# Performance work log

Hardware: AMD Instinct MI355X
Metric: run time of the kernel (lower is better)

Reference implementation:

```python
import jax, jax.numpy as jnp
import numpy as np

N_NODES = 100000
N_EDGES = 1600000
D_IN = 128
D_OUT = 128
K_HOPS = 2


def gcn_norm(edge_index, num_nodes):
    # Add self-loops (weight 1), compute symmetric normalization
    # norm_e = deg^{-1/2}[src] * deg^{-1/2}[dst], deg over destination index.
    loop = jnp.arange(num_nodes, dtype=edge_index.dtype)
    src = jnp.concatenate([edge_index[0], loop])
    dst = jnp.concatenate([edge_index[1], loop])
    w = jnp.ones(src.shape[0], dtype=jnp.float32)
    deg = jax.ops.segment_sum(w, dst, num_segments=num_nodes)
    dinv = jnp.where(deg > 0, jax.lax.rsqrt(deg), 0.0)
    norm = dinv[src] * dinv[dst]
    return src, dst, norm


def setup_inputs() -> dict:
    key = jax.random.key(0)
    k1, k2, k3, k4 = jax.random.split(key, 4)
    x = jax.random.normal(k1, (N_NODES, D_IN), dtype=jnp.float32)
    edge_index = jax.random.randint(k2, (2, N_EDGES), 0, N_NODES, dtype=jnp.int64)
    # SGConv linear params (Glorot-ish scale)
    W = jax.random.normal(k3, (D_IN, D_OUT), dtype=jnp.float32) / np.sqrt(D_IN)
    b = jnp.zeros((D_OUT,), dtype=jnp.float32)
    return {"x": x, "edge_index": edge_index, "W": W, "b": b}


def reference(x, edge_index, W, b):
    n = x.shape[0]
    src, dst, norm = gcn_norm(edge_index, n)
    h = x
    for _ in range(K_HOPS):
        # gather source features, scale by edge norm, scatter-add to destinations
        h = jax.ops.segment_sum(h[src] * norm[:, None], dst, num_segments=n)
    return h @ W + b
```

## Files before the change

kernel.cpp:

```cpp
#include <hip/hip_runtime.h>
#include <hip/hip_bf16.h>


#define DFEAT 128
#define ELLW 64
#define ABLK 2048
#define CAP 4608
#define NBUCKMAX 512

typedef __attribute__((ext_vector_type(8))) short short8;
typedef __attribute__((ext_vector_type(4))) float f32x4;
typedef __attribute__((ext_vector_type(4))) unsigned int u32x4;
typedef __attribute__((ext_vector_type(4))) int i32x4;

__device__ __forceinline__ float bf2f(unsigned short u) {
    union { unsigned int i; float f; } t;
    t.i = ((unsigned int)u) << 16;
    return t.f;
}

__device__ __forceinline__ unsigned short f2bf(float f) {
    union { float f; unsigned int i; } t;
    t.f = f;
    unsigned int lsb = (t.i >> 16) & 1u;
    t.i += 0x7fffu + lsb;
    return (unsigned short)(t.i >> 16);
}

__device__ __forceinline__ void accum8(float* acc, uint4 u, float w) {
    acc[0] += bf2f((unsigned short)(u.x & 0xffffu)) * w;
    acc[1] += bf2f((unsigned short)(u.x >> 16)) * w;
    acc[2] += bf2f((unsigned short)(u.y & 0xffffu)) * w;
    acc[3] += bf2f((unsigned short)(u.y >> 16)) * w;
    acc[4] += bf2f((unsigned short)(u.z & 0xffffu)) * w;
    acc[5] += bf2f((unsigned short)(u.z >> 16)) * w;
    acc[6] += bf2f((unsigned short)(u.w & 0xffffu)) * w;
    acc[7] += bf2f((unsigned short)(u.w >> 16)) * w;
}

__device__ __forceinline__ void add8(float* acc, uint4 u) {
    union { unsigned int i; float f; } a;
    a.i = u.x << 16;          acc[0] += a.f;
    a.i = u.x & 0xffff0000u;  acc[1] += a.f;
    a.i = u.y << 16;          acc[2] += a.f;
    a.i = u.y & 0xffff0000u;  acc[3] += a.f;
    a.i = u.z << 16;          acc[4] += a.f;
    a.i = u.z & 0xffff0000u;  acc[5] += a.f;
    a.i = u.w << 16;          acc[6] += a.f;
    a.i = u.w & 0xffff0000u;  acc[7] += a.f;
}

__global__ void k_detect(const unsigned short* __restrict__ xs,
                         const int* __restrict__ ei, int* __restrict__ flags) {
    int t = blockIdx.x * 256 + (int)threadIdx.x;
    int bad = 0;
    for (int i = t; i < 16384; i += 2048) {
        unsigned int e = (xs[i] >> 7) & 0xFFu;
        if (e >= 0xC0u) bad = 1;
    }
    if (__any(bad) && (threadIdx.x & 63) == 0) atomicOr(flags, 1);
    int oddnz = 0;
    for (int i = t; i < 4096; i += 2048) {
        if (ei[2 * i + 1] != 0) oddnz = 1;
    }
    if (__any(oddnz) && (threadIdx.x & 63) == 0) atomicOr(flags + 1, 1);
}

__global__ void k_prepB(const void* __restrict__ Wraw, const int* __restrict__ flags,
                        unsigned short* __restrict__ Bf) {
    int t = blockIdx.x * 256 + threadIdx.x;
    if (t >= 2048) return;
    int lane = t & 63;
    int chunk = (t >> 6) & 3;
    int ntile = t >> 8;
    int ncol = ntile * 16 + (lane & 15);
    int k0 = chunk * 32 + (lane >> 4) * 8;
    int isf = flags[0];
    const float* Wf = (const float*)Wraw;
    const unsigned short* Wb = (const unsigned short*)Wraw;
    unsigned short* o = Bf + (size_t)t * 8;
#pragma unroll
    for (int j = 0; j < 8; j++) {
        int idx = (k0 + j) * DFEAT + ncol;
        o[j] = isf ? f2bf(Wf[idx]) : Wb[idx];
    }
}

__global__ __launch_bounds__(256) void k_bucketA(const int* __restrict__ ei, int E, int n,
                                                 const int* __restrict__ flags,
                                                 int* __restrict__ bucketCnt,
                                                 unsigned int* __restrict__ buck) {
    __shared__ int sdst[ABLK];
    __shared__ int ssrc[ABLK];
    __shared__ int hist[NBUCKMAX];
    __shared__ int base_[NBUCKMAX];
    int tid = (int)threadIdx.x;
    for (int t = tid; t < NBUCKMAX; t += 256) hist[t] = 0;
    __syncthreads();
    int e0 = blockIdx.x * ABLK;
    int i64 = (flags[1] == 0);

    if (e0 + ABLK <= E) {
        int d[8], s[8];
#pragma unroll
        for (int k = 0; k < 8; k++) {
            int e = e0 + tid + k * 256;
            d[k] = i64 ? __builtin_nontemporal_load(ei + 2 * (E + e))
                       : __builtin_nontemporal_load(ei + E + e);
        }
#pragma unroll
        for (int k = 0; k < 8; k++) {
            int e = e0 + tid + k * 256;
            s[k] = i64 ? __builtin_nontemporal_load(ei + 2 * e)
                       : __builtin_nontemporal_load(ei + e);
        }
#pragma unroll
        for (int k = 0; k < 8; k++) {
            sdst[tid + k * 256] = d[k];
            ssrc[tid + k * 256] = s[k];
            atomicAdd(&hist[d[k] >> 8], 1);
        }
    } else {
        for (int e = e0 + tid; e < E; e += 256) {
            int d = i64 ? ei[2 * (E + e)] : ei[E + e];
            int s = i64 ? ei[2 * e] : ei[e];
            sdst[e - e0] = d;
            ssrc[e - e0] = s;
            atomicAdd(&hist[d >> 8], 1);
        }
    }
    __syncthreads();
#pragma unroll
    for (int r = 0; r < 2; r++) {
        int t = (tid + r * 256 + (int)blockIdx.x * 61) & (NBUCKMAX - 1);
        int cc = hist[t];
        base_[t] = cc ? atomicAdd(bucketCnt + t, cc) : 0;
        hist[t] = 0;
    }
    __syncthreads();
    int nloc = min(ABLK, E - e0);
    if (nloc == ABLK) {
#pragma unroll
        for (int k = 0; k < 8; k++) {
            int idx = tid + k * 256;
            int d = sdst[idx], s = ssrc[idx];
            int b = d >> 8;
            int pos = base_[b] + atomicAdd(&hist[b], 1);
            if (pos < CAP)
                buck[(size_t)b * CAP + pos] =
                    (unsigned int)s | ((unsigned int)(d & 255) << 17);
        }
    } else {
        for (int idx = tid; idx < nloc; idx += 256) {
            int d = sdst[idx], s = ssrc[idx];
            int b = d >> 8;
            int pos = base_[b] + atomicAdd(&hist[b], 1);
            if (pos < CAP)
                buck[(size_t)b * CAP + pos] =
                    (unsigned int)s | ((unsigned int)(d & 255) << 17);
        }
    }
}

__global__ __launch_bounds__(256) void k_bucketB_gemm0(
        const unsigned int* __restrict__ buck,
        const int* __restrict__ bucketCnt, int n,
        int* __restrict__ cnt, int* __restrict__ ell,
        const void* __restrict__ xraw,
        const unsigned short* __restrict__ Bf,
        const int* __restrict__ flags,
        unsigned short* __restrict__ g0) {
    __shared__ int lcnt[256];
    __shared__ unsigned short thi[16 * 136];
    __shared__ unsigned short tlo[16 * 136];
    int b = blockIdx.x;
    int tid = (int)threadIdx.x;
    lcnt[tid] = 0;
    __syncthreads();

    int m0 = min(bucketCnt[b], CAP);
    int node0 = b << 8;
    const unsigned int* bp = buck + (size_t)b * CAP;
    for (int base = 0; base < m0; base += 1024) {
        unsigned int w[4];
#pragma unroll
        for (int j = 0; j < 4; j++) {
            int i = base + tid + j * 256;
            w[j] = (i < m0) ? __builtin_nontemporal_load(bp + i) : 0xFFFFFFFFu;
        }
#pragma unroll
        for (int j = 0; j < 4; j++) {
            if (w[j] != 0xFFFFFFFFu) {
                int s = (int)(w[j] & 0x1FFFFu);
                int dl = (int)(w[j] >> 17);
                int pos = atomicAdd(&lcnt[dl], 1);
                if (pos < ELLW) ell[(size_t)(node0 + dl) * ELLW + pos] = s;
            }
        }
    }
    __syncthreads();
    {
        int node = node0 + tid;
        if (node < n) {
            int c = lcnt[tid];
            cnt[node] = c;
            int st = min(c, ELLW);
            int slots = min((c + 16) & ~15, ELLW);
            int* rowp = ell + (size_t)node * ELLW;
            for (int p = st; p < slots; p++) rowp[p] = node;
        }
    }

    int isf = flags[0];
    int wave = tid >> 6;
    int lane = tid & 63;
    int g = lane >> 4, c = lane & 15;
    int trow = wave * 4 + g;

    for (int tile = 0; tile < 16; ++tile) {
        int lrow = tile * 16 + trow;
        int node = node0 + lrow;
        uint4 ohi = {0, 0, 0, 0}, olo = {0, 0, 0, 0};
        if (node < n) {
            if (isf) {
                const float* xf = (const float*)xraw;
                f32x4 v0 = __builtin_nontemporal_load((const f32x4*)(xf + (size_t)node * DFEAT + c * 8));
                f32x4 v1 = __builtin_nontemporal_load((const f32x4*)(xf + (size_t)node * DFEAT + c * 8 + 4));
                float vv[8] = {v0[0], v0[1], v0[2], v0[3], v1[0], v1[1], v1[2], v1[3]};
                unsigned short h[8], l[8];
#pragma unroll
                for (int j = 0; j < 8; j++) {
                    h[j] = f2bf(vv[j]);
                    l[j] = f2bf(vv[j] - bf2f(h[j]));
                }
                ohi.x = (unsigned int)h[0] | ((unsigned int)h[1] << 16);
                ohi.y = (unsigned int)h[2] | ((unsigned int)h[3] << 16);
                ohi.z = (unsigned int)h[4] | ((unsigned int)h[5] << 16);
                ohi.w = (unsigned int)h[6] | ((unsigned int)h[7] << 16);
                olo.x = (unsigned int)l[0] | ((unsigned int)l[1] << 16);
                olo.y = (unsigned int)l[2] | ((unsigned int)l[3] << 16);
                olo.z = (unsigned int)l[4] | ((unsigned int)l[5] << 16);
                olo.w = (unsigned int)l[6] | ((unsigned int)l[7] << 16);
            } else {
                u32x4 u = __builtin_nontemporal_load(
                    (const u32x4*)((const unsigned short*)xraw + (size_t)node * DFEAT + c * 8));
                ohi.x = u[0]; ohi.y = u[1]; ohi.z = u[2]; ohi.w = u[3];
            }
        }
        __syncthreads();
        *(uint4*)(thi + trow * 136 + c * 8) = ohi;
        *(uint4*)(tlo + trow * 136 + c * 8) = olo;
        __syncthreads();

        int m = c, quad = g;
        f32x4 acc2[2];
        acc2[0] = (f32x4){0.f, 0.f, 0.f, 0.f};
        acc2[1] = (f32x4){0.f, 0.f, 0.f, 0.f};
#pragma unroll
        for (int c2 = 0; c2 < 4; c2++) {
            short8 ah = *(const short8*)(thi + m * 136 + c2 * 32 + quad * 8);
            short8 al = *(const short8*)(tlo + m * 136 + c2 * 32 + quad * 8);
#pragma unroll
            for (int t = 0; t < 2; t++) {
                int nt = wave * 2 + t;
                short8 bfr = *(const short8*)(Bf + ((size_t)(nt * 4 + c2) * 64 + lane) * 8);
                acc2[t] = __builtin_amdgcn_mfma_f32_16x16x32_bf16(ah, bfr, acc2[t], 0, 0, 0);
                acc2[t] = __builtin_amdgcn_mfma_f32_16x16x32_bf16(al, bfr, acc2[t], 0, 0, 0);
            }
        }

        float sc[4];
#pragma unroll
        for (int r2 = 0; r2 < 4; r2++) {
            int lr = tile * 16 + quad * 4 + r2;
            sc[r2] = (node0 + lr < n) ? rsqrtf((float)(lcnt[lr] + 1)) : 0.f;
        }
#pragma unroll
        for (int t = 0; t < 2; t++) {
            int col = (wave * 2 + t) * 16 + m;
#pragma unroll
            for (int r2 = 0; r2 < 4; r2++) {
                int gnode = node0 + tile * 16 + quad * 4 + r2;
                if (gnode < n)
                    g0[(size_t)gnode * DFEAT + col] = f2bf(acc2[t][r2] * sc[r2]);
            }
        }
    }
}

__device__ __forceinline__ void hop_accum(const unsigned short* __restrict__ fb,
                                          const int* __restrict__ ell,
                                          int node, int cn, int lane, float* acc) {
    int g = lane >> 4, c = lane & 15;
    int slots = min((cn + 16) & ~15, ELLW);
    const int* row = ell + (size_t)node * ELLW;
#pragma unroll
    for (int j = 0; j < 8; j++) acc[j] = 0.f;

    for (int base = 0; base < slots; base += 16) {
        i32x4 s4 = __builtin_nontemporal_load((const i32x4*)(row + base) + g);
        uint4 u0 = *(const uint4*)(fb + (size_t)s4[0] * DFEAT + c * 8);
        uint4 u1 = *(const uint4*)(fb + (size_t)s4[1] * DFEAT + c * 8);
        uint4 u2 = *(const uint4*)(fb + (size_t)s4[2] * DFEAT + c * 8);
        uint4 u3 = *(const uint4*)(fb + (size_t)s4[3] * DFEAT + c * 8);
        add8(acc, u0);
        add8(acc, u1);
        add8(acc, u2);
        add8(acc, u3);
    }
    float corrw = (cn < ELLW) ? (float)(cn + 1 - slots) : 1.0f;
    if (g == 0 && corrw != 0.0f) {
        uint4 u = *(const uint4*)(fb + (size_t)node * DFEAT + c * 8);
        accum8(acc, u, corrw);
    }
#pragma unroll
    for (int j = 0; j < 8; j++) {
        acc[j] += __shfl_xor(acc[j], 16);
        acc[j] += __shfl_xor(acc[j], 32);
    }
}

__global__ __launch_bounds__(256) void k_hop(const unsigned short* __restrict__ src,
                                             const int* __restrict__ ell,
                                             const int* __restrict__ cnt,
                                             unsigned short* __restrict__ outb, int n) {
    int node = blockIdx.x * 4 + (threadIdx.x >> 6);
    if (node >= n) return;
    int lane = threadIdx.x & 63;
    int cn = cnt[node];
    float acc[8];
    hop_accum(src, ell, node, cn, lane, acc);
    if ((lane >> 4) == 0) {
        int c = lane & 15;
        float sc = 1.0f / (float)(cn + 1);
        uint4 o;
        o.x = (unsigned int)f2bf(acc[0] * sc) | ((unsigned int)f2bf(acc[1] * sc) << 16);
        o.y = (unsigned int)f2bf(acc[2] * sc) | ((unsigned int)f2bf(acc[3] * sc) << 16);
        o.z = (unsigned int)f2bf(acc[4] * sc) | ((unsigned int)f2bf(acc[5] * sc) << 16);
        o.w = (unsigned int)f2bf(acc[6] * sc) | ((unsigned int)f2bf(acc[7] * sc) << 16);
        *(uint4*)(outb + (size_t)node * DFEAT + c * 8) = o;
    }
}

__global__ __launch_bounds__(256) void k_hop2_out(const unsigned short* __restrict__ src,
                                                  const int* __restrict__ ell,
                                                  const int* __restrict__ cnt,
                                                  const void* __restrict__ braw,
                                                  const int* __restrict__ flags,
                                                  void* __restrict__ outraw, int n) {
    int node = blockIdx.x * 4 + (threadIdx.x >> 6);
    if (node >= n) return;
    int lane = threadIdx.x & 63;
    int cn = cnt[node];
    float acc[8];
    hop_accum(src, ell, node, cn, lane, acc);
    if ((lane >> 4) == 0) {
        int c = lane & 15;
        float sc = rsqrtf((float)(cn + 1));
        int isf = flags[0];
        const float* bf32 = (const float*)braw;
        const unsigned short* bb16 = (const unsigned short*)braw;
#pragma unroll
        for (int j = 0; j < 8; j++) {
            float bias = isf ? bf32[c * 8 + j] : bf2f(bb16[c * 8 + j]);
            acc[j] = acc[j] * sc + bias;
        }
        if (isf) {
            float* outf = (float*)outraw;
            *(float4*)(outf + (size_t)node * DFEAT + c * 8) =
                (float4){acc[0], acc[1], acc[2], acc[3]};
            *(float4*)(outf + (size_t)node * DFEAT + c * 8 + 4) =
                (float4){acc[4], acc[5], acc[6], acc[7]};
        } else {
            unsigned short* outb = (unsigned short*)outraw;
            uint4 o;
            o.x = (unsigned int)f2bf(acc[0]) | ((unsigned int)f2bf(acc[1]) << 16);
            o.y = (unsigned int)f2bf(acc[2]) | ((unsigned int)f2bf(acc[3]) << 16);
            o.z = (unsigned int)f2bf(acc[4]) | ((unsigned int)f2bf(acc[5]) << 16);
            o.w = (unsigned int)f2bf(acc[6]) | ((unsigned int)f2bf(acc[7]) << 16);
            *(uint4*)(outb + (size_t)node * DFEAT + c * 8) = o;
        }
    }
}

extern "C" void kernel_launch(void* const* d_in, const int* in_sizes, int n_in,
                              void* d_out, int out_size, void* d_ws, size_t ws_size,
                              hipStream_t stream) {
    const void* x = d_in[0];
    const int* ei = (const int*)d_in[1];
    const void* W = d_in[2];
    const void* b = d_in[3];

    const int n = in_sizes[0] / DFEAT;
    const int E = in_sizes[1] / 2;

    int* ell = (int*)d_ws;
    unsigned short* g1 = (unsigned short*)(ell + (size_t)n * ELLW);
    int* cnt = (int*)(g1 + (size_t)n * DFEAT);
    int* flags = cnt + n;
    int* bucketCnt = flags + 4;
    unsigned short* Bf = (unsigned short*)(bucketCnt + NBUCKMAX);
    unsigned short* g0 = (unsigned short*)d_out;
    unsigned int* buck = (unsigned int*)g1;

    (void)hipMemsetAsync(flags, 0, (4 + NBUCKMAX) * sizeof(int), stream);

    k_detect<<<8, 256, 0, stream>>>((const unsigned short*)x, ei, flags);

    k_prepB<<<8, 256, 0, stream>>>(W, flags, Bf);

    int nbuck = (n + 255) >> 8;
    int ablocks = (E + ABLK - 1) / ABLK;
    k_bucketA<<<ablocks, 256, 0, stream>>>(ei, E, n, flags, bucketCnt, buck);

    k_bucketB_gemm0<<<nbuck, 256, 0, stream>>>(buck, bucketCnt, n, cnt, ell,
                                               x, Bf, flags, g0);

    k_hop<<<(n + 3) / 4, 256, 0, stream>>>(g0, ell, cnt, g1, n);

    k_hop2_out<<<(n + 3) / 4, 256, 0, stream>>>(g1, ell, cnt, b, flags, d_out, n);
}
```

Baseline: 308.1 us.

## Locally sort edges by bucket before scatter and merge setup kernels

The bucketing kernel now processes 4096 edges per block, builds a per-block prefix scan over bucket histograms, and locally sorts edge indices by destination bucket in shared memory. Global writes to bucket arrays then become contiguous runs per bucket, which should coalesce better. Separately, the memset, dtype-detect and W-prep launches are merged into a single one-block setup kernel to cut launch overhead. The cost is more shared-memory passes and barriers, plus fewer resident blocks from the larger LDS footprint.

Result: slower. 324.7 us (+5.4%).

```diff
diff --git a/kernel.cpp b/kernel.cpp
--- a/kernel.cpp
+++ b/kernel.cpp
@@ -4,7 +4,7 @@
 
 #define DFEAT 128
 #define ELLW 64
-#define ABLK 2048
+#define ABLK 4096
 #define CAP 4608
 #define NBUCKMAX 512
 
@@ -50,39 +50,46 @@
     a.i = u.w & 0xffff0000u;  acc[7] += a.f;
 }
 
-__global__ void k_detect(const unsigned short* __restrict__ xs,
-                         const int* __restrict__ ei, int* __restrict__ flags) {
-    int t = blockIdx.x * 256 + (int)threadIdx.x;
+__global__ __launch_bounds__(256) void k_setup(const unsigned short* __restrict__ xs,
+                                               const int* __restrict__ ei,
+                                               const void* __restrict__ Wraw,
+                                               int* __restrict__ flags,
+                                               int* __restrict__ bucketCnt,
+                                               unsigned short* __restrict__ Bf) {
+    __shared__ int s_f32, s_odd;
+    int tid = (int)threadIdx.x;
+    if (tid == 0) { s_f32 = 0; s_odd = 0; }
+    for (int i = tid; i < NBUCKMAX; i += 256) bucketCnt[i] = 0;
+    __syncthreads();
     int bad = 0;
-    for (int i = t; i < 16384; i += 2048) {
+    for (int i = tid; i < 16384; i += 256) {
         unsigned int e = (xs[i] >> 7) & 0xFFu;
         if (e >= 0xC0u) bad = 1;
     }
-    if (__any(bad) && (threadIdx.x & 63) == 0) atomicOr(flags, 1);
-    int oddnz = 0;
-    for (int i = t; i < 4096; i += 2048) {
-        if (ei[2 * i + 1] != 0) oddnz = 1;
-    }
-    if (__any(oddnz) && (threadIdx.x & 63) == 0) atomicOr(flags + 1, 1);
-}
-
-__global__ void k_prepB(const void* __restrict__ Wraw, const int* __restrict__ flags,
-                        unsigned short* __restrict__ Bf) {
-    int t = blockIdx.x * 256 + threadIdx.x;
-    if (t >= 2048) return;
-    int lane = t & 63;
-    int chunk = (t >> 6) & 3;
-    int ntile = t >> 8;
-    int ncol = ntile * 16 + (lane & 15);
-    int k0 = chunk * 32 + (lane >> 4) * 8;
-    int isf = flags[0];
+    if (bad) atomicOr(&s_f32, 1);
+    int odd = 0;
+    for (int i = tid; i < 4096; i += 256) {
+        if (ei[2 * i + 1] != 0) odd = 1;
+    }
+    if (odd) atomicOr(&s_odd, 1);
+    __syncthreads();
+    int isf = s_f32;
+    if (tid == 0) { flags[0] = s_f32; flags[1] = s_odd; }
+
     const float* Wf = (const float*)Wraw;
     const unsigned short* Wb = (const unsigned short*)Wraw;
-    unsigned short* o = Bf + (size_t)t * 8;
-#pragma unroll
-    for (int j = 0; j < 8; j++) {
-        int idx = (k0 + j) * DFEAT + ncol;
-        o[j] = isf ? f2bf(Wf[idx]) : Wb[idx];
+    for (int t = tid; t < 2048; t += 256) {
+        int lane = t & 63;
+        int chunk = (t >> 6) & 3;
+        int ntile = t >> 8;
+        int ncol = ntile * 16 + (lane & 15);
+        int k0 = chunk * 32 + (lane >> 4) * 8;
+        unsigned short* o = Bf + (size_t)t * 8;
+#pragma unroll
+        for (int j = 0; j < 8; j++) {
+            int idx = (k0 + j) * DFEAT + ncol;
+            o[j] = isf ? f2bf(Wf[idx]) : Wb[idx];
+        }
     }
 }
 
@@ -90,75 +97,74 @@
                                                  const int* __restrict__ flags,
                                                  int* __restrict__ bucketCnt,
                                                  unsigned int* __restrict__ buck) {
-    __shared__ int sdst[ABLK];
+    __shared__ int sd[ABLK];
     __shared__ int ssrc[ABLK];
+    __shared__ unsigned short sidx[ABLK];
     __shared__ int hist[NBUCKMAX];
-    __shared__ int base_[NBUCKMAX];
+    __shared__ int loff[NBUCKMAX];
+    __shared__ int gbase[NBUCKMAX];
+    __shared__ int cur[NBUCKMAX];
+    __shared__ int scan_s[256];
+
     int tid = (int)threadIdx.x;
     for (int t = tid; t < NBUCKMAX; t += 256) hist[t] = 0;
     __syncthreads();
     int e0 = blockIdx.x * ABLK;
+    int nloc = min(ABLK, E - e0);
     int i64 = (flags[1] == 0);
 
-    if (e0 + ABLK <= E) {
-        int d[8], s[8];
-#pragma unroll
-        for (int k = 0; k < 8; k++) {
-            int e = e0 + tid + k * 256;
-            d[k] = i64 ? __builtin_nontemporal_load(ei + 2 * (E + e))
-                       : __builtin_nontemporal_load(ei + E + e);
-        }
-#pragma unroll
-        for (int k = 0; k < 8; k++) {
-            int e = e0 + tid + k * 256;
-            s[k] = i64 ? __builtin_nontemporal_load(ei + 2 * e)
-                       : __builtin_nontemporal_load(ei + e);
-        }
-#pragma unroll
-        for (int k = 0; k < 8; k++) {
-            sdst[tid + k * 256] = d[k];
-            ssrc[tid + k * 256] = s[k];
-            atomicAdd(&hist[d[k] >> 8], 1);
-        }
-    } else {
-        for (int e = e0 + tid; e < E; e += 256) {
-            int d = i64 ? ei[2 * (E + e)] : ei[E + e];
-            int s = i64 ? ei[2 * e] : ei[e];
-            sdst[e - e0] = d;
-            ssrc[e - e0] = s;
-            atomicAdd(&hist[d >> 8], 1);
-        }
-    }
-    __syncthreads();
+    for (int i = tid; i < nloc; i += 256) {
+        int e = e0 + i;
+        int d = i64 ? __builtin_nontemporal_load(ei + 2 * (E + e))
+                    : __builtin_nontemporal_load(ei + E + e);
+        int s = i64 ? __builtin_nontemporal_load(ei + 2 * e)
+                    : __builtin_nontemporal_load(ei + e);
+        sd[i] = d;
+        ssrc[i] = s;
+    }
+    __syncthreads();
+
+    for (int i = tid; i < nloc; i += 256) atomicAdd(&hist[sd[i] >> 8], 1);
+    __syncthreads();
+
+    int a0 = hist[2 * tid], a1 = hist[2 * tid + 1];
+    int pair = a0 + a1;
+    scan_s[tid] = pair;
+    __syncthreads();
+    for (int off = 1; off < 256; off <<= 1) {
+        int t = (tid >= off) ? scan_s[tid - off] : 0;
+        __syncthreads();
+        scan_s[tid] += t;
+        __syncthreads();
+    }
+    int ex = scan_s[tid] - pair;
+    loff[2 * tid] = ex;
+    loff[2 * tid + 1] = ex + a0;
+
 #pragma unroll
     for (int r = 0; r < 2; r++) {
         int t = (tid + r * 256 + (int)blockIdx.x * 61) & (NBUCKMAX - 1);
         int cc = hist[t];
-        base_[t] = cc ? atomicAdd(bucketCnt + t, cc) : 0;
-        hist[t] = 0;
-    }
-    __syncthreads();
-    int nloc = min(ABLK, E - e0);
-    if (nloc == ABLK) {
-#pragma unroll
-        for (int k = 0; k < 8; k++) {
-            int idx = tid + k * 256;
-            int d = sdst[idx], s = ssrc[idx];
-            int b = d >> 8;
-            int pos = base_[b] + atomicAdd(&hist[b], 1);
-            if (pos < CAP)
-                buck[(size_t)b * CAP + pos] =
-                    (unsigned int)s | ((unsigned int)(d & 255) << 17);
-        }
-    } else {
-        for (int idx = tid; idx < nloc; idx += 256) {
-            int d = sdst[idx], s = ssrc[idx];
-            int b = d >> 8;
-            int pos = base_[b] + atomicAdd(&hist[b], 1);
-            if (pos < CAP)
-                buck[(size_t)b * CAP + pos] =
-                    (unsigned int)s | ((unsigned int)(d & 255) << 17);
-        }
+        gbase[t] = cc ? atomicAdd(bucketCnt + t, cc) : 0;
+        cur[t] = 0;
+    }
+    __syncthreads();
+
+    for (int i = tid; i < nloc; i += 256) {
+        int b = sd[i] >> 8;
+        int p = loff[b] + atomicAdd(&cur[b], 1);
+        sidx[p] = (unsigned short)i;
+    }
+    __syncthreads();
+
+    for (int i = tid; i < nloc; i += 256) {
+        int idx = sidx[i];
+        int d = sd[idx];
+        int b = d >> 8;
+        int pos = gbase[b] + (i - loff[b]);
+        if (pos < CAP)
+            buck[(size_t)b * CAP + pos] =
+                (unsigned int)ssrc[idx] | ((unsigned int)(d & 255) << 17);
     }
 }
 
@@ -403,11 +409,8 @@
     unsigned short* g0 = (unsigned short*)d_out;
     unsigned int* buck = (unsigned int*)g1;
 
-    (void)hipMemsetAsync(flags, 0, (4 + NBUCKMAX) * sizeof(int), stream);
-
-    k_detect<<<8, 256, 0, stream>>>((const unsigned short*)x, ei, flags);
-
-    k_prepB<<<8, 256, 0, stream>>>(W, flags, Bf);
+    k_setup<<<1, 256, 0, stream>>>((const unsigned short*)x, ei, W,
+                                   flags, bucketCnt, Bf);
 
     int nbuck = (n + 255) >> 8;
     int ablocks = (E + ABLK - 1) / ABLK;
```
